# Optimization experiments

Hardware: AMD Instinct MI355X
Metric: run time of the kernel (lower is better)

The kernel has to match this reference:

```python
import jax, jax.numpy as jnp
import numpy as np

B, S, H, I, E, TOP_K = 2, 1024, 1024, 2048, 8, 2


def setup_inputs() -> dict:
    key = jax.random.key(0)
    k1, k2, k3, k4 = jax.random.split(key, 4)
    return {
        "hidden_states": jax.random.normal(k1, (B, S, H), dtype=jnp.float32),
        "gate_weight": jax.random.normal(k2, (E, H), dtype=jnp.float32) * 0.02,
        "gate_up_proj": jax.random.normal(k3, (E, 2 * I, H), dtype=jnp.float32) * 0.02,
        "down_proj": jax.random.normal(k4, (E, H, I), dtype=jnp.float32) * 0.02,
    }


def reference(hidden_states, gate_weight, gate_up_proj, down_proj):
    b, s, h = hidden_states.shape
    T = b * s
    x = hidden_states.reshape(T, h)

    # --- router ---
    router_logits = x @ gate_weight.T                          # [T, E]
    router_probs = jax.nn.softmax(router_logits.astype(jnp.float32), axis=-1)
    router_probs = router_probs.astype(router_logits.dtype)
    top_vals, top_idx = jax.lax.top_k(router_probs, TOP_K)     # [T, K]
    # norm_topk_prob = True
    routing_weights = top_vals / jnp.maximum(top_vals.sum(-1, keepdims=True), 1e-12)

    # --- dense all-expert FFN ---
    gu = jnp.einsum('th,eoh->eto', x, gate_up_proj)            # [E, T, 2I]
    gate_h, up_h = jnp.split(gu, 2, axis=-1)
    inter = jax.nn.silu(gate_h) * up_h                          # [E, T, I]
    expert_out = jnp.einsum('eti,ehi->eth', inter, down_proj).astype(jnp.float32)  # [E, T, H]

    # --- pairwise Frobenius similarity (sim = 1 - dist/max_dist, diag=1) ---
    flat = expert_out.reshape(E, -1)
    gram = flat @ flat.T                                        # [E, E]
    sq = jnp.diagonal(gram)
    dist = jnp.sqrt(jnp.clip(sq[:, None] + sq[None, :] - 2.0 * gram, 0.0))
    dist = dist.at[jnp.arange(E), jnp.arange(E)].set(0.0)
    sim = 1.0 - dist / jnp.maximum(dist.max(), 1e-12)
    sim = sim.at[jnp.arange(E), jnp.arange(E)].set(1.0)

    # --- top-k weighted combine (gather along expert axis) ---
    gathered = expert_out[top_idx, jnp.arange(T)[:, None]]      # [T, K, H]
    final = (gathered * routing_weights[..., None].astype(jnp.float32)).sum(axis=1)
    final = final.astype(hidden_states.dtype).reshape(b, s, h)
    return final, sim
```

## Files before the change

### kernel.cpp

```cpp
#include <hip/hip_runtime.h>
#include <math.h>

#define T_TOK 2048
#define H_DIM 1024
#define I_DIM 2048
#define NEXP  8

typedef _Float16 f16x8 __attribute__((ext_vector_type(8)));
typedef _Float16 f16x4 __attribute__((ext_vector_type(4)));
typedef float    f32x4 __attribute__((ext_vector_type(4)));

__device__ __forceinline__ void cp16(const void* g, void* l) {
  __builtin_amdgcn_global_load_lds(
      (const __attribute__((address_space(1))) void*)g,
      (__attribute__((address_space(3))) void*)l, 16, 0, 0);
}

__global__ __launch_bounds__(256) void cvt_f16_kernel(
    const float* __restrict__ in, _Float16* __restrict__ hi, int n) {
  int i = (blockIdx.x * 256 + threadIdx.x) * 4;
  if (i >= n) return;
  float4 v = *(const float4*)(in + i);
  f16x4 hv = {(_Float16)v.x, (_Float16)v.y, (_Float16)v.z, (_Float16)v.w};
  *(f16x4*)(hi + i) = hv;
}

__global__ __launch_bounds__(64) void router_kernel(
    const float* __restrict__ x, const float* __restrict__ gw,
    int* __restrict__ topIdx, float* __restrict__ topW) {
  int t = blockIdx.x;
  int lane = threadIdx.x;
  float p[NEXP];
#pragma unroll
  for (int e = 0; e < NEXP; ++e) p[e] = 0.f;
  const float* xr = x + (size_t)t * H_DIM;
  for (int h = lane; h < H_DIM; h += 64) {
    float xv = xr[h];
#pragma unroll
    for (int e = 0; e < NEXP; ++e) p[e] += xv * gw[e * H_DIM + h];
  }
#pragma unroll
  for (int e = 0; e < NEXP; ++e) {
    float v = p[e];
    for (int off = 32; off > 0; off >>= 1) v += __shfl_down(v, off);
    p[e] = v;
  }
  if (lane == 0) {
    float mx = p[0];
#pragma unroll
    for (int e = 1; e < NEXP; ++e) mx = fmaxf(mx, p[e]);
    float ex[NEXP], s = 0.f;
#pragma unroll
    for (int e = 0; e < NEXP; ++e) { ex[e] = expf(p[e] - mx); s += ex[e]; }
#pragma unroll
    for (int e = 0; e < NEXP; ++e) ex[e] /= s;
    int i0 = 0; float v0 = ex[0];
#pragma unroll
    for (int e = 1; e < NEXP; ++e) if (ex[e] > v0) { v0 = ex[e]; i0 = e; }
    int i1 = -1; float v1 = -1.f;
#pragma unroll
    for (int e = 0; e < NEXP; ++e) if (e != i0 && ex[e] > v1) { v1 = ex[e]; i1 = e; }
    float sum = fmaxf(v0 + v1, 1e-12f);
    topIdx[2 * t] = i0;  topIdx[2 * t + 1] = i1;
    topW[2 * t] = v0 / sum;  topW[2 * t + 1] = v1 / sum;
  }
}

__global__ __launch_bounds__(256, 2) void gemm_gateup(
    const _Float16* __restrict__ xHi, const _Float16* __restrict__ gup16,
    _Float16* __restrict__ intHi) {
  __shared__ _Float16 lds[12288];

  const int tid = threadIdx.x;
  const int wave = tid >> 6, lane = tid & 63;
  const int rowA0 = blockIdx.y * 128;
  const int colB0 = blockIdx.x * 128;
  const int e = blockIdx.z;

  const int r0 = tid >> 2;
  const int s0 = tid & 3;
  const int swr = (r0 ^ (r0 >> 2)) & 3;
  const int g0 = s0 ^ swr;

  const int wm = wave >> 1, wn = wave & 1;
  const int fr = lane & 15;
  const int quad = lane >> 4;
  const int swf = (fr ^ (fr >> 2)) & 3;
  const int fk = (quad ^ swf) * 8;

  f32x4 accG[4][4], accU[4][4];
#pragma unroll
  for (int i = 0; i < 4; ++i)
#pragma unroll
    for (int j = 0; j < 4; ++j) {
      accG[i][j] = (f32x4){0.f, 0.f, 0.f, 0.f};
      accU[i][j] = (f32x4){0.f, 0.f, 0.f, 0.f};
    }

  const _Float16* gupG = gup16 + ((size_t)e * 2 * I_DIM + colB0) * H_DIM;
  const _Float16* gupU = gupG + (size_t)I_DIM * H_DIM;
  char* ldsB = (char*)lds;

  for (int k0 = 0; k0 < H_DIM; k0 += 32) {
    const int kcol = k0 + g0 * 8;
    cp16(xHi + (size_t)(rowA0 + r0) * H_DIM + kcol, ldsB + wave * 1024u);
    cp16(xHi + (size_t)(rowA0 + r0 + 64) * H_DIM + kcol, ldsB + 4096u + wave * 1024u);
    cp16(gupG + (size_t)r0 * H_DIM + kcol, ldsB + 8192u + wave * 1024u);
    cp16(gupG + (size_t)(r0 + 64) * H_DIM + kcol, ldsB + 12288u + wave * 1024u);
    cp16(gupU + (size_t)r0 * H_DIM + kcol, ldsB + 16384u + wave * 1024u);
    cp16(gupU + (size_t)(r0 + 64) * H_DIM + kcol, ldsB + 20480u + wave * 1024u);
    __syncthreads();

    f16x8 ah[4];
#pragma unroll
    for (int i = 0; i < 4; ++i)
      ah[i] = *(const f16x8*)&lds[(wm * 64 + i * 16 + fr) * 32 + fk];
#pragma unroll
    for (int j = 0; j < 4; ++j) {
      const int boff = (wn * 64 + j * 16 + fr) * 32 + fk;
      f16x8 bg = *(const f16x8*)&lds[4096 + boff];
      f16x8 bu = *(const f16x8*)&lds[8192 + boff];
#pragma unroll
      for (int i = 0; i < 4; ++i) {
        accG[i][j] = __builtin_amdgcn_mfma_f32_16x16x32_f16(ah[i], bg, accG[i][j], 0, 0, 0);
        accU[i][j] = __builtin_amdgcn_mfma_f32_16x16x32_f16(ah[i], bu, accU[i][j], 0, 0, 0);
      }
    }
    __syncthreads();
  }

  const int er = quad * 4;
  const int ec = lane & 15;
#pragma unroll
  for (int i = 0; i < 4; ++i)
#pragma unroll
    for (int j = 0; j < 4; ++j) {
      const int row = rowA0 + wm * 64 + i * 16 + er;
      const int col = colB0 + wn * 64 + j * 16 + ec;
#pragma unroll
      for (int r = 0; r < 4; ++r) {
        float g = accG[i][j][r], u = accU[i][j][r];
        float val = g / (1.f + __expf(-g)) * u;
        intHi[((size_t)e * T_TOK + row + r) * I_DIM + col] = (_Float16)val;
      }
    }
}

__global__ __launch_bounds__(256, 4) void gemm_down(
    const _Float16* __restrict__ intHi, const _Float16* __restrict__ wd16,
    _Float16* __restrict__ eo) {
  __shared__ _Float16 lds[8192];

  const int tid = threadIdx.x;
  const int wave = tid >> 6, lane = tid & 63;
  const int rowA0 = blockIdx.x * 128;
  const int colB0 = blockIdx.y * 128;
  const int e = blockIdx.z;

  const int r0 = tid >> 2;
  const int s0 = tid & 3;
  const int swr = (r0 ^ (r0 >> 2)) & 3;
  const int g0 = s0 ^ swr;

  const int wm = wave >> 1, wn = wave & 1;
  const int fr = lane & 15;
  const int quad = lane >> 4;
  const int swf = (fr ^ (fr >> 2)) & 3;
  const int fk = (quad ^ swf) * 8;

  f32x4 acc[4][4];
#pragma unroll
  for (int i = 0; i < 4; ++i)
#pragma unroll
    for (int j = 0; j < 4; ++j) acc[i][j] = (f32x4){0.f, 0.f, 0.f, 0.f};

  const _Float16* aBase = intHi + (size_t)e * T_TOK * I_DIM;
  const _Float16* bBase = wd16 + ((size_t)e * H_DIM + colB0) * I_DIM;
  char* ldsB = (char*)lds;

  for (int k0 = 0; k0 < I_DIM; k0 += 32) {
    const int kcol = k0 + g0 * 8;
    cp16(aBase + (size_t)(rowA0 + r0) * I_DIM + kcol, ldsB + wave * 1024u);
    cp16(aBase + (size_t)(rowA0 + r0 + 64) * I_DIM + kcol, ldsB + 4096u + wave * 1024u);
    cp16(bBase + (size_t)(r0) * I_DIM + kcol, ldsB + 8192u + wave * 1024u);
    cp16(bBase + (size_t)(r0 + 64) * I_DIM + kcol, ldsB + 12288u + wave * 1024u);
    __syncthreads();

    f16x8 ah[4];
#pragma unroll
    for (int i = 0; i < 4; ++i)
      ah[i] = *(const f16x8*)&lds[(wm * 64 + i * 16 + fr) * 32 + fk];
#pragma unroll
    for (int j = 0; j < 4; ++j) {
      const int boff = (wn * 64 + j * 16 + fr) * 32 + fk;
      f16x8 bh = *(const f16x8*)&lds[4096 + boff];
#pragma unroll
      for (int i = 0; i < 4; ++i)
        acc[i][j] = __builtin_amdgcn_mfma_f32_16x16x32_f16(ah[i], bh, acc[i][j], 0, 0, 0);
    }
    __syncthreads();
  }

  const int er = quad * 4;
  const int ec = lane & 15;
#pragma unroll
  for (int i = 0; i < 4; ++i)
#pragma unroll
    for (int j = 0; j < 4; ++j) {
      const int row = rowA0 + wm * 64 + i * 16 + er;
      const int col = colB0 + wn * 64 + j * 16 + ec;
#pragma unroll
      for (int r = 0; r < 4; ++r)
        eo[((size_t)e * T_TOK + row + r) * H_DIM + col] = (_Float16)acc[i][j][r];
    }
}

__global__ __launch_bounds__(256) void gram_kernel(
    const _Float16* __restrict__ eo, float* __restrict__ gram) {
  float s[36];
#pragma unroll
  for (int p = 0; p < 36; ++p) s[p] = 0.f;
  const size_t total = (size_t)T_TOK * H_DIM;
  const size_t stride = (size_t)gridDim.x * 256;
  for (size_t j = (size_t)blockIdx.x * 256 + threadIdx.x; j < total; j += stride) {
    float v[NEXP];
#pragma unroll
    for (int e = 0; e < NEXP; ++e) v[e] = (float)eo[(size_t)e * total + j];
    int p = 0;
#pragma unroll
    for (int a = 0; a < NEXP; ++a)
#pragma unroll
      for (int b = a; b < NEXP; ++b) { s[p] += v[a] * v[b]; ++p; }
  }
#pragma unroll
  for (int p = 0; p < 36; ++p) {
    float v = s[p];
    for (int off = 32; off > 0; off >>= 1) v += __shfl_down(v, off);
    s[p] = v;
  }
  __shared__ float red[4][36];
  const int wave = threadIdx.x >> 6, lane = threadIdx.x & 63;
  if (lane == 0)
#pragma unroll
    for (int p = 0; p < 36; ++p) red[wave][p] = s[p];
  __syncthreads();
  if (threadIdx.x < 36) {
    float v = red[0][threadIdx.x] + red[1][threadIdx.x] + red[2][threadIdx.x] + red[3][threadIdx.x];
    atomicAdd(&gram[threadIdx.x], v);
  }
}

__global__ __launch_bounds__(64) void sim_kernel(
    const float* __restrict__ gram, float* __restrict__ simOut) {
  const int t = threadIdx.x;
  const int e1 = t >> 3, e2 = t & 7;
  int a = e1 < e2 ? e1 : e2;
  int b = e1 < e2 ? e2 : e1;
  const float g = gram[a * 8 - a * (a - 1) / 2 + (b - a)];
  const float sq1 = gram[e1 * 8 - e1 * (e1 - 1) / 2];
  const float sq2 = gram[e2 * 8 - e2 * (e2 - 1) / 2];
  float d2 = fmaxf(sq1 + sq2 - 2.f * g, 0.f);
  float dist = (e1 == e2) ? 0.f : sqrtf(d2);
  float dmax = dist;
  for (int off = 32; off > 0; off >>= 1) dmax = fmaxf(dmax, __shfl_xor(dmax, off));
  float sim = 1.f - dist / fmaxf(dmax, 1e-12f);
  if (e1 == e2) sim = 1.f;
  simOut[t] = sim;
}

__global__ __launch_bounds__(256) void final_kernel(
    const _Float16* __restrict__ eo, const int* __restrict__ topIdx,
    const float* __restrict__ topW, float* __restrict__ out) {
  const int t = blockIdx.x;
  const int c = threadIdx.x * 4;
  const int i0 = topIdx[2 * t], i1 = topIdx[2 * t + 1];
  const float w0 = topW[2 * t], w1 = topW[2 * t + 1];
  const size_t per = (size_t)T_TOK * H_DIM;
  f16x4 a = *(const f16x4*)&eo[(size_t)i0 * per + (size_t)t * H_DIM + c];
  f16x4 b = *(const f16x4*)&eo[(size_t)i1 * per + (size_t)t * H_DIM + c];
  float4 r;
  r.x = w0 * (float)a[0] + w1 * (float)b[0];
  r.y = w0 * (float)a[1] + w1 * (float)b[1];
  r.z = w0 * (float)a[2] + w1 * (float)b[2];
  r.w = w0 * (float)a[3] + w1 * (float)b[3];
  *(float4*)&out[(size_t)t * H_DIM + c] = r;
}

extern "C" void kernel_launch(void* const* d_in, const int* in_sizes, int n_in,
                              void* d_out, int out_size, void* d_ws, size_t ws_size,
                              hipStream_t stream) {
  (void)in_sizes; (void)n_in; (void)out_size; (void)ws_size;
  const float* x   = (const float*)d_in[0];
  const float* gw  = (const float*)d_in[1];
  const float* gup = (const float*)d_in[2];
  const float* dwn = (const float*)d_in[3];
  float* out = (float*)d_out;

  char* ws = (char*)d_ws;
  const size_t MB = 1u << 20;
  _Float16* xHi    = (_Float16*)(ws + 0 * MB);
  _Float16* intHi  = (_Float16*)(ws + 4 * MB);
  _Float16* gup16  = (_Float16*)(ws + 68 * MB);
  _Float16* wd16   = (_Float16*)(ws + 68 * MB);
  _Float16* eo     = (_Float16*)(ws + 100 * MB);
  int*      topIdx = (int*)(ws + 132 * MB);
  float*    topW   = (float*)(ws + 132 * MB + 16384);
  float*    gram   = (float*)(ws + 132 * MB + 32768);

  cvt_f16_kernel<<<2048, 256, 0, stream>>>(x, xHi, T_TOK * H_DIM);
  cvt_f16_kernel<<<32768, 256, 0, stream>>>(gup, gup16, NEXP * 2 * I_DIM * H_DIM);
  router_kernel<<<T_TOK, 64, 0, stream>>>(x, gw, topIdx, topW);
  hipMemsetAsync(gram, 0, 36 * sizeof(float), stream);

  gemm_gateup<<<dim3(I_DIM / 128, T_TOK / 128, NEXP), 256, 0, stream>>>(
      xHi, gup16, intHi);

  cvt_f16_kernel<<<16384, 256, 0, stream>>>(dwn, wd16, NEXP * H_DIM * I_DIM);

  gemm_down<<<dim3(T_TOK / 128, H_DIM / 128, NEXP), 256, 0, stream>>>(
      intHi, wd16, eo);

  gram_kernel<<<2048, 256, 0, stream>>>(eo, gram);
  sim_kernel<<<1, 64, 0, stream>>>(gram, out + (size_t)T_TOK * H_DIM);
  final_kernel<<<T_TOK, 256, 0, stream>>>(eo, topIdx, topW, out);
}
```

Measured before the change: 548.5 us.

## Double K-tile depth to 64 with XOR-swizzled LDS layout in both GEMMs

Both expert GEMMs now stage a K-slice of 64 instead of 32 per iteration, which halves the number of barrier pairs and loop iterations over K. The shared tile is laid out as 64-element rows with an 8-way XOR swizzle on both the load and fragment-read side to avoid LDS bank conflicts. LDS use doubles to 48KB and 32KB per block, which may reduce occupancy. There is still no double buffering, so global loads and MFMA work do not overlap.

```diff
diff --git a/kernel.cpp b/kernel.cpp
--- a/kernel.cpp
+++ b/kernel.cpp
@@ -69,7 +69,7 @@
 __global__ __launch_bounds__(256, 2) void gemm_gateup(
     const _Float16* __restrict__ xHi, const _Float16* __restrict__ gup16,
     _Float16* __restrict__ intHi) {
-  __shared__ _Float16 lds[12288];
+  __shared__ _Float16 lds[24576];
 
   const int tid = threadIdx.x;
   const int wave = tid >> 6, lane = tid & 63;
@@ -77,16 +77,14 @@
   const int colB0 = blockIdx.x * 128;
   const int e = blockIdx.z;
 
-  const int r0 = tid >> 2;
-  const int s0 = tid & 3;
-  const int swr = (r0 ^ (r0 >> 2)) & 3;
-  const int g0 = s0 ^ swr;
+  const int sr = lane >> 3;
+  const int sc = lane & 7;
+  const int gcol = (sc ^ sr) * 8;
+  const int rbase = wave * 8 + sr;
 
   const int wm = wave >> 1, wn = wave & 1;
   const int fr = lane & 15;
   const int quad = lane >> 4;
-  const int swf = (fr ^ (fr >> 2)) & 3;
-  const int fk = (quad ^ swf) * 8;
 
   f32x4 accG[4][4], accU[4][4];
 #pragma unroll
@@ -101,29 +99,37 @@
   const _Float16* gupU = gupG + (size_t)I_DIM * H_DIM;
   char* ldsB = (char*)lds;
 
-  for (int k0 = 0; k0 < H_DIM; k0 += 32) {
-    const int kcol = k0 + g0 * 8;
-    cp16(xHi + (size_t)(rowA0 + r0) * H_DIM + kcol, ldsB + wave * 1024u);
-    cp16(xHi + (size_t)(rowA0 + r0 + 64) * H_DIM + kcol, ldsB + 4096u + wave * 1024u);
-    cp16(gupG + (size_t)r0 * H_DIM + kcol, ldsB + 8192u + wave * 1024u);
-    cp16(gupG + (size_t)(r0 + 64) * H_DIM + kcol, ldsB + 12288u + wave * 1024u);
-    cp16(gupU + (size_t)r0 * H_DIM + kcol, ldsB + 16384u + wave * 1024u);
-    cp16(gupU + (size_t)(r0 + 64) * H_DIM + kcol, ldsB + 20480u + wave * 1024u);
+  for (int k0 = 0; k0 < H_DIM; k0 += 64) {
+    const int kcol = k0 + gcol;
+#pragma unroll
+    for (int i = 0; i < 4; ++i) {
+      const int row = i * 32 + rbase;
+      const unsigned dst = (unsigned)(i * 4096 + wave * 1024);
+      cp16(xHi  + (size_t)(rowA0 + row) * H_DIM + kcol, ldsB + dst);
+      cp16(gupG + (size_t)row * H_DIM + kcol, ldsB + 16384u + dst);
+      cp16(gupU + (size_t)row * H_DIM + kcol, ldsB + 32768u + dst);
+    }
     __syncthreads();
 
-    f16x8 ah[4];
-#pragma unroll
-    for (int i = 0; i < 4; ++i)
-      ah[i] = *(const f16x8*)&lds[(wm * 64 + i * 16 + fr) * 32 + fk];
-#pragma unroll
-    for (int j = 0; j < 4; ++j) {
-      const int boff = (wn * 64 + j * 16 + fr) * 32 + fk;
-      f16x8 bg = *(const f16x8*)&lds[4096 + boff];
-      f16x8 bu = *(const f16x8*)&lds[8192 + boff];
+#pragma unroll
+    for (int kk = 0; kk < 2; ++kk) {
+      f16x8 ah[4];
 #pragma unroll
       for (int i = 0; i < 4; ++i) {
-        accG[i][j] = __builtin_amdgcn_mfma_f32_16x16x32_f16(ah[i], bg, accG[i][j], 0, 0, 0);
-        accU[i][j] = __builtin_amdgcn_mfma_f32_16x16x32_f16(ah[i], bu, accU[i][j], 0, 0, 0);
+        const int row = wm * 64 + i * 16 + fr;
+        ah[i] = *(const f16x8*)&lds[row * 64 + (((kk * 4 + quad) ^ (fr & 7)) * 8)];
+      }
+#pragma unroll
+      for (int j = 0; j < 4; ++j) {
+        const int row = wn * 64 + j * 16 + fr;
+        const int boff = row * 64 + (((kk * 4 + quad) ^ (fr & 7)) * 8);
+        f16x8 bg = *(const f16x8*)&lds[8192 + boff];
+        f16x8 bu = *(const f16x8*)&lds[16384 + boff];
+#pragma unroll
+        for (int i = 0; i < 4; ++i) {
+          accG[i][j] = __builtin_amdgcn_mfma_f32_16x16x32_f16(ah[i], bg, accG[i][j], 0, 0, 0);
+          accU[i][j] = __builtin_amdgcn_mfma_f32_16x16x32_f16(ah[i], bu, accU[i][j], 0, 0, 0);
+        }
       }
     }
     __syncthreads();
@@ -149,7 +155,7 @@
 __global__ __launch_bounds__(256, 4) void gemm_down(
     const _Float16* __restrict__ intHi, const _Float16* __restrict__ wd16,
     _Float16* __restrict__ eo) {
-  __shared__ _Float16 lds[8192];
+  __shared__ _Float16 lds[16384];
 
   const int tid = threadIdx.x;
   const int wave = tid >> 6, lane = tid & 63;
@@ -157,16 +163,14 @@
   const int colB0 = blockIdx.y * 128;
   const int e = blockIdx.z;
 
-  const int r0 = tid >> 2;
-  const int s0 = tid & 3;
-  const int swr = (r0 ^ (r0 >> 2)) & 3;
-  const int g0 = s0 ^ swr;
+  const int sr = lane >> 3;
+  const int sc = lane & 7;
+  const int gcol = (sc ^ sr) * 8;
+  const int rbase = wave * 8 + sr;
 
   const int wm = wave >> 1, wn = wave & 1;
   const int fr = lane & 15;
   const int quad = lane >> 4;
-  const int swf = (fr ^ (fr >> 2)) & 3;
-  const int fk = (quad ^ swf) * 8;
 
   f32x4 acc[4][4];
 #pragma unroll
@@ -178,25 +182,34 @@
   const _Float16* bBase = wd16 + ((size_t)e * H_DIM + colB0) * I_DIM;
   char* ldsB = (char*)lds;
 
-  for (int k0 = 0; k0 < I_DIM; k0 += 32) {
-    const int kcol = k0 + g0 * 8;
-    cp16(aBase + (size_t)(rowA0 + r0) * I_DIM + kcol, ldsB + wave * 1024u);
-    cp16(aBase + (size_t)(rowA0 + r0 + 64) * I_DIM + kcol, ldsB + 4096u + wave * 1024u);
-    cp16(bBase + (size_t)(r0) * I_DIM + kcol, ldsB + 8192u + wave * 1024u);
-    cp16(bBase + (size_t)(r0 + 64) * I_DIM + kcol, ldsB + 12288u + wave * 1024u);
+  for (int k0 = 0; k0 < I_DIM; k0 += 64) {
+    const int kcol = k0 + gcol;
+#pragma unroll
+    for (int i = 0; i < 4; ++i) {
+      const int row = i * 32 + rbase;
+      const unsigned dst = (unsigned)(i * 4096 + wave * 1024);
+      cp16(aBase + (size_t)(rowA0 + row) * I_DIM + kcol, ldsB + dst);
+      cp16(bBase + (size_t)row * I_DIM + kcol, ldsB + 16384u + dst);
+    }
     __syncthreads();
 
-    f16x8 ah[4];
-#pragma unroll
-    for (int i = 0; i < 4; ++i)
-      ah[i] = *(const f16x8*)&lds[(wm * 64 + i * 16 + fr) * 32 + fk];
-#pragma unroll
-    for (int j = 0; j < 4; ++j) {
-      const int boff = (wn * 64 + j * 16 + fr) * 32 + fk;
-      f16x8 bh = *(const f16x8*)&lds[4096 + boff];
-#pragma unroll
-      for (int i = 0; i < 4; ++i)
-        acc[i][j] = __builtin_amdgcn_mfma_f32_16x16x32_f16(ah[i], bh, acc[i][j], 0, 0, 0);
+#pragma unroll
+    for (int kk = 0; kk < 2; ++kk) {
+      f16x8 ah[4];
+#pragma unroll
+      for (int i = 0; i < 4; ++i) {
+        const int row = wm * 64 + i * 16 + fr;
+        ah[i] = *(const f16x8*)&lds[row * 64 + (((kk * 4 + quad) ^ (fr & 7)) * 8)];
+      }
+#pragma unroll
+      for (int j = 0; j < 4; ++j) {
+        const int row = wn * 64 + j * 16 + fr;
+        const int boff = row * 64 + (((kk * 4 + quad) ^ (fr & 7)) * 8);
+        f16x8 bh = *(const f16x8*)&lds[8192 + boff];
+#pragma unroll
+        for (int i = 0; i < 4; ++i)
+          acc[i][j] = __builtin_amdgcn_mfma_f32_16x16x32_f16(ah[i], bh, acc[i][j], 0, 0, 0);
+      }
     }
     __syncthreads();
   }
```

After: 506.9 us. -7.6%, faster.
